# Kernel tuning notes

Hardware: AMD Instinct MI355X
Metric: run time of the kernel (lower is better)

## Reference

```python
import jax, jax.numpy as jnp
import numpy as np

B, S, D, H = 2, 2048, 1024, 16
DH = D // H
NEG = jnp.float32(-1e30)


def setup_inputs() -> dict:
    key = jax.random.key(0)
    ks = jax.random.split(key, 5)
    x = jax.random.normal(ks[0], (B, S, D), dtype=jnp.float32)
    # causal mask: attn_mask == 0 means blocked (matches masked_fill(attn_mask == 0))
    attn_mask = jnp.tril(jnp.ones((S, S), dtype=jnp.int32))
    key_padding_mask = jnp.zeros((B, S), dtype=bool)  # True = pad (none here)
    sd = 1.0 / np.sqrt(D)
    W_qkv = jax.random.normal(ks[1], (D, 3 * D), dtype=jnp.float32) * sd
    b_qkv = jnp.zeros((3 * D,), dtype=jnp.float32)
    W_proj = jax.random.normal(ks[2], (D, D), dtype=jnp.float32) * sd
    b_proj = jnp.zeros((D,), dtype=jnp.float32)
    return {"x": x, "W_qkv": W_qkv, "b_qkv": b_qkv, "W_proj": W_proj,
            "b_proj": b_proj, "attn_mask": attn_mask,
            "key_padding_mask": key_padding_mask}


def reference(x, W_qkv, b_qkv, W_proj, b_proj, attn_mask, key_padding_mask):
    scale = jnp.float32(DH) ** -0.5
    qkv = (x @ W_qkv + b_qkv).reshape(B, S, 3, H, DH)
    qkv = jnp.transpose(qkv, (2, 0, 3, 1, 4))  # (3, B, H, S, DH)
    q, k, v = qkv[0], qkv[1], qkv[2]
    attn = jnp.einsum("bhqd,bhkd->bhqk", q, k) * scale  # (B,H,S,S)
    # key padding mask: True -> -inf on that key column
    attn = jnp.where(key_padding_mask[:, None, None, :], NEG, attn)
    # attn mask: 0 -> blocked
    attn = jnp.where(attn_mask[None, None, :, :] == 0, NEG, attn)
    attn = jax.nn.softmax(attn, axis=-1)
    out = jnp.einsum("bhqk,bhkd->bhqd", attn, v)
    out = jnp.transpose(out, (0, 2, 1, 3)).reshape(B, S, D)
    return out @ W_proj + b_proj
```

## Files before the change

### kernel.cpp

```cpp
#include <hip/hip_runtime.h>


typedef __bf16 bf16;
typedef bf16 bf16x4 __attribute__((ext_vector_type(4)));
typedef bf16 bf16x8 __attribute__((ext_vector_type(8)));
typedef float f32x4 __attribute__((ext_vector_type(4)));

#define S_LEN 2048
#define DMODEL 1024
#define NHEAD 16
#define DHEAD 64

__device__ __forceinline__ void async_ld16(void* lds, const void* g) {
  __builtin_amdgcn_global_load_lds(
      (const __attribute__((address_space(1))) unsigned int*)g,
      (__attribute__((address_space(3))) unsigned int*)lds, 16, 0, 0);
}

__global__ __launch_bounds__(256) void prep_kernel(
    const float* __restrict__ x, const float* __restrict__ Wq,
    const float* __restrict__ Wp, bf16* __restrict__ Xb,
    bf16* __restrict__ Wtq, bf16* __restrict__ Wtp) {
  __shared__ float t[32][33];
  const int bid = blockIdx.x, tid = threadIdx.x;
  if (bid < 4096) {
    int i = bid * 256 + tid;
    float4 v = ((const float4*)x)[i];
    bf16x4 o;
    o[0] = (bf16)v.x; o[1] = (bf16)v.y; o[2] = (bf16)v.z; o[3] = (bf16)v.w;
    *(bf16x4*)(&Xb[4 * i]) = o;
    return;
  }
  const float* in; bf16* out; int R, C, bx, by;
  if (bid < 7168) {
    int b = bid - 4096; in = Wq; out = Wtq; R = 1024; C = 3072;
    bx = b % 96; by = b / 96;
  } else {
    int b = bid - 7168; in = Wp; out = Wtp; R = 1024; C = 1024;
    bx = b % 32; by = b / 32;
  }
  int tx = tid & 31, ty = tid >> 5;
  int bc = bx * 32, br = by * 32;
#pragma unroll
  for (int i = 0; i < 32; i += 8)
    t[ty + i][tx] = in[(size_t)(br + ty + i) * C + bc + tx];
  __syncthreads();
#pragma unroll
  for (int i = 0; i < 32; i += 8)
    out[(size_t)(bc + ty + i) * R + br + tx] = (bf16)t[tx][ty + i];
}

__global__ __launch_bounds__(512) void gemm_qkv(
    const bf16* __restrict__ A, const bf16* __restrict__ Bt,
    const float* __restrict__ bias, bf16* __restrict__ Oq,
    bf16* __restrict__ Ok, bf16* __restrict__ Ov, int Ksz) {
  __shared__ bf16 As[256 * 32];
  __shared__ bf16 Bs[128 * 32];
  const int tid = threadIdx.x, lane = tid & 63, w = tid >> 6;
  const int wm = (w >> 1) * 64, wn = (w & 1) * 64;
  const int lr = lane & 15, kg = lane >> 4;
  const int m0 = blockIdx.y * 256, n0 = blockIdx.x * 128;

  f32x4 acc[4][4] = {};

  bf16x8 areg[2], breg;
  const int ar0 = (tid) >> 2,        ac0 = (tid & 3) * 8;
  const int ar1 = (tid + 512) >> 2,  ac1 = ((tid + 512) & 3) * 8;
  const int br_ = tid >> 2,          bc_ = (tid & 3) * 8;

  areg[0] = *(const bf16x8*)(&A[(size_t)(m0 + ar0) * Ksz + ac0]);
  areg[1] = *(const bf16x8*)(&A[(size_t)(m0 + ar1) * Ksz + ac1]);
  breg    = *(const bf16x8*)(&Bt[(size_t)(n0 + br_) * Ksz + bc_]);

  for (int k0 = 0; k0 < Ksz; k0 += 32) {
    *(bf16x8*)(&As[ar0 * 32 + ac0]) = areg[0];
    *(bf16x8*)(&As[ar1 * 32 + ac1]) = areg[1];
    *(bf16x8*)(&Bs[br_ * 32 + bc_]) = breg;
    __syncthreads();

    if (k0 + 32 < Ksz) {
      const int kn = k0 + 32;
      areg[0] = *(const bf16x8*)(&A[(size_t)(m0 + ar0) * Ksz + kn + ac0]);
      areg[1] = *(const bf16x8*)(&A[(size_t)(m0 + ar1) * Ksz + kn + ac1]);
      breg    = *(const bf16x8*)(&Bt[(size_t)(n0 + br_) * Ksz + kn + bc_]);
    }

    bf16x8 af[4], bfr[4];
#pragma unroll
    for (int i = 0; i < 4; ++i)
      af[i] = *(const bf16x8*)(&As[(wm + i * 16 + lr) * 32 + kg * 8]);
#pragma unroll
    for (int j = 0; j < 4; ++j)
      bfr[j] = *(const bf16x8*)(&Bs[(wn + j * 16 + lr) * 32 + kg * 8]);
#pragma unroll
    for (int i = 0; i < 4; ++i)
#pragma unroll
      for (int j = 0; j < 4; ++j)
        acc[i][j] = __builtin_amdgcn_mfma_f32_16x16x32_bf16(af[i], bfr[j], acc[i][j], 0, 0, 0);
    __syncthreads();
  }

  const int rbase = kg * 4;
  const int t = n0 >> 10;
  if (t == 2) {
#pragma unroll
    for (int i = 0; i < 4; ++i) {
#pragma unroll
      for (int j = 0; j < 4; ++j) {
        int ncol = n0 + wn + j * 16 + lr;
        float bv = bias[ncol];
        int rem = ncol & 1023, h = rem >> 6, d = rem & 63;
        int m = m0 + wm + i * 16 + rbase;
        int s = m & 2047;
        size_t hb = (size_t)((m >> 11) * NHEAD + h) * S_LEN;
        bf16x4 pk;
#pragma unroll
        for (int r = 0; r < 4; ++r) pk[r] = (bf16)(acc[i][j][r] + bv);
        *(bf16x4*)(&Ov[hb * DHEAD + (size_t)d * S_LEN + s]) = pk;
      }
    }
  } else {
    bf16* Oqk = (t == 0) ? Oq : Ok;
#pragma unroll
    for (int i = 0; i < 4; ++i) {
#pragma unroll
      for (int j = 0; j < 4; ++j) {
        int ncol = n0 + wn + j * 16 + lr;
        float bv = bias[ncol];
        int rem = ncol & 1023, h = rem >> 6, d = rem & 63;
#pragma unroll
        for (int r = 0; r < 4; ++r) {
          int m = m0 + wm + i * 16 + rbase + r;
          int s = m & 2047;
          size_t hb = (size_t)((m >> 11) * NHEAD + h) * S_LEN;
          Oqk[(hb + s) * DHEAD + d] = (bf16)(acc[i][j][r] + bv);
        }
      }
    }
  }
}

__global__ __launch_bounds__(256) void gemm_proj(
    const bf16* __restrict__ A, const bf16* __restrict__ Bt,
    const float* __restrict__ bias, float* __restrict__ Of,
    int Ksz, int Nsz) {
  __shared__ bf16 As[64 * 32];
  __shared__ bf16 Bs[128 * 32];
  const int tid = threadIdx.x, lane = tid & 63, w = tid >> 6;
  const int wm = (w >> 1) * 32, wn = (w & 1) * 64;
  const int lr = lane & 15, kg = lane >> 4;
  const int m0 = blockIdx.y * 64, n0 = blockIdx.x * 128;

  f32x4 acc[2][4] = {};

  bf16x8 areg, breg[2];
  const int ar_ = tid >> 2,          ac_ = (tid & 3) * 8;
  const int br0 = tid >> 2,          bc0 = (tid & 3) * 8;
  const int br1 = (tid + 256) >> 2,  bc1 = ((tid + 256) & 3) * 8;

  areg    = *(const bf16x8*)(&A[(size_t)(m0 + ar_) * Ksz + ac_]);
  breg[0] = *(const bf16x8*)(&Bt[(size_t)(n0 + br0) * Ksz + bc0]);
  breg[1] = *(const bf16x8*)(&Bt[(size_t)(n0 + br1) * Ksz + bc1]);

  for (int k0 = 0; k0 < Ksz; k0 += 32) {
    *(bf16x8*)(&As[ar_ * 32 + ac_]) = areg;
    *(bf16x8*)(&Bs[br0 * 32 + bc0]) = breg[0];
    *(bf16x8*)(&Bs[br1 * 32 + bc1]) = breg[1];
    __syncthreads();

    if (k0 + 32 < Ksz) {
      const int kn = k0 + 32;
      areg    = *(const bf16x8*)(&A[(size_t)(m0 + ar_) * Ksz + kn + ac_]);
      breg[0] = *(const bf16x8*)(&Bt[(size_t)(n0 + br0) * Ksz + kn + bc0]);
      breg[1] = *(const bf16x8*)(&Bt[(size_t)(n0 + br1) * Ksz + kn + bc1]);
    }

    bf16x8 af[2], bfr[4];
#pragma unroll
    for (int i = 0; i < 2; ++i)
      af[i] = *(const bf16x8*)(&As[(wm + i * 16 + lr) * 32 + kg * 8]);
#pragma unroll
    for (int j = 0; j < 4; ++j)
      bfr[j] = *(const bf16x8*)(&Bs[(wn + j * 16 + lr) * 32 + kg * 8]);
#pragma unroll
    for (int i = 0; i < 2; ++i)
#pragma unroll
      for (int j = 0; j < 4; ++j)
        acc[i][j] = __builtin_amdgcn_mfma_f32_16x16x32_bf16(af[i], bfr[j], acc[i][j], 0, 0, 0);
    __syncthreads();
  }

  const int rbase = kg * 4;
#pragma unroll
  for (int i = 0; i < 2; ++i) {
#pragma unroll
    for (int j = 0; j < 4; ++j) {
      int ncol = n0 + wn + j * 16 + lr;
      float bv = bias[ncol];
#pragma unroll
      for (int r = 0; r < 4; ++r) {
        int m = m0 + wm + i * 16 + rbase + r;
        Of[(size_t)m * Nsz + ncol] = acc[i][j][r] + bv;
      }
    }
  }
}

__global__ __launch_bounds__(256) void attn_kernel(
    const bf16* __restrict__ Q, const bf16* __restrict__ K,
    const bf16* __restrict__ Vtg, bf16* __restrict__ O) {
  __shared__ bf16 Ks[128 * 72];
  __shared__ bf16 Vt[80 * 136];

  const int tid = threadIdx.x, lane = tid & 63, w = tid >> 6;
  const int lr = lane & 15, quad = lane >> 4;
  const int flat = blockIdx.x;
  const int p = (flat >> 3) & 15;
  const int bh = (flat & 7) + ((flat >> 7) << 3);
  const int b = bh >> 4, h = bh & 15;
  const bf16* Qp = Q + (size_t)bh * S_LEN * DHEAD;
  const bf16* Kp = K + (size_t)bh * S_LEN * DHEAD;
  const bf16* Vp = Vtg + (size_t)bh * S_LEN * DHEAD;

  for (int i = tid; i < 16 * 136; i += 256) {
    int rr = i / 136;
    Vt[(64 + rr) * 136 + (i - rr * 136)] = (rr == 0) ? (bf16)1.0f : (bf16)0.0f;
  }
  __syncthreads();

  const float qs = 0.125f * 1.44269504f;

  for (int seg = 0; seg < 2; ++seg) {
    const int qt = seg ? (31 - p) : p;
    const int q0 = qt * 64;
    const int qrow = q0 + w * 16;

    bf16x8 q0r = *(const bf16x8*)(Qp + (size_t)(qrow + lr) * DHEAD + quad * 8);
    bf16x8 q1r = *(const bf16x8*)(Qp + (size_t)(qrow + lr) * DHEAD + 32 + quad * 8);
    bf16x8 qf0, qf1;
#pragma unroll
    for (int e = 0; e < 8; ++e) {
      qf0[e] = (bf16)((float)q0r[e] * qs);
      qf1[e] = (bf16)((float)q1r[e] * qs);
    }

    f32x4 acc[4] = {};
    f32x4 acc5 = {};

    const int ktiles = (q0 + 63) / 128 + 1;

    bf16x8 kreg[4], vreg[4];
#pragma unroll
    for (int i = 0; i < 4; ++i) {
      int sg = tid + i * 256;
      int krow = sg >> 3, kc = (sg & 7) * 8;
      kreg[i] = *(const bf16x8*)(&Kp[(size_t)krow * DHEAD + kc]);
      int vd = sg >> 4, vs = (sg & 15) * 8;
      vreg[i] = *(const bf16x8*)(&Vp[(size_t)vd * S_LEN + vs]);
    }

    for (int kt = 0; kt < ktiles; ++kt) {
      const int kb = kt * 128;
#pragma unroll
      for (int i = 0; i < 4; ++i) {
        int sg = tid + i * 256;
        int krow = sg >> 3, kc = (sg & 7) * 8;
        int kl = krow & 31;
        int Rrow = (krow & ~31) | (((kl >> 2) & 1) << 4) | (((kl >> 3) & 3) << 2) | (kl & 3);
        *(bf16x8*)(&Ks[Rrow * 72 + kc]) = kreg[i];
        int vd = sg >> 4, vs = (sg & 15) * 8;
        *(bf16x8*)(&Vt[vd * 136 + vs]) = vreg[i];
      }
      __syncthreads();

      if (kt + 1 < ktiles) {
        const int kbn = kb + 128;
#pragma unroll
        for (int i = 0; i < 4; ++i) {
          int sg = tid + i * 256;
          int krow = sg >> 3, kc = (sg & 7) * 8;
          kreg[i] = *(const bf16x8*)(&Kp[(size_t)(kbn + krow) * DHEAD + kc]);
          int vd = sg >> 4, vs = (sg & 15) * 8;
          vreg[i] = *(const bf16x8*)(&Vp[(size_t)vd * S_LEN + kbn + vs]);
        }
      }

      f32x4 sc[8];
      __builtin_amdgcn_s_setprio(1);
#pragma unroll
      for (int ct = 0; ct < 8; ++ct) {
        bf16x8 kf0 = *(const bf16x8*)(&Ks[(ct * 16 + lr) * 72 + quad * 8]);
        bf16x8 kf1 = *(const bf16x8*)(&Ks[(ct * 16 + lr) * 72 + 32 + quad * 8]);
        f32x4 a = {};
        a = __builtin_amdgcn_mfma_f32_16x16x32_bf16(kf0, qf0, a, 0, 0, 0);
        a = __builtin_amdgcn_mfma_f32_16x16x32_bf16(kf1, qf1, a, 0, 0, 0);
        sc[ct] = a;
      }
      __builtin_amdgcn_s_setprio(0);

      if ((kb + 127) > qrow) {
        const int qg = qrow + lr;
#pragma unroll
        for (int ct = 0; ct < 8; ++ct)
#pragma unroll
          for (int r = 0; r < 4; ++r) {
            int key = kb + (ct >> 1) * 32 + quad * 8 + (ct & 1) * 4 + r;
            if (key > qg) sc[ct][r] = -1e30f;
          }
      }

      bf16x8 p8[4];
#pragma unroll
      for (int k0 = 0; k0 < 4; ++k0) {
        bf16x8 pf;
#pragma unroll
        for (int c = 0; c < 2; ++c)
#pragma unroll
          for (int r = 0; r < 4; ++r)
            pf[c * 4 + r] = (bf16)__builtin_amdgcn_exp2f(sc[2 * k0 + c][r]);
        p8[k0] = pf;
      }

      __builtin_amdgcn_s_setprio(1);
#pragma unroll
      for (int k0 = 0; k0 < 4; ++k0) {
#pragma unroll
        for (int nt = 0; nt < 4; ++nt) {
          bf16x8 vf = *(const bf16x8*)(&Vt[(nt * 16 + lr) * 136 + k0 * 32 + quad * 8]);
          acc[nt] = __builtin_amdgcn_mfma_f32_16x16x32_bf16(vf, p8[k0], acc[nt], 0, 0, 0);
        }
        bf16x8 vf5 = *(const bf16x8*)(&Vt[(64 + lr) * 136 + k0 * 32 + quad * 8]);
        acc5 = __builtin_amdgcn_mfma_f32_16x16x32_bf16(vf5, p8[k0], acc5, 0, 0, 0);
      }
      __builtin_amdgcn_s_setprio(0);
      __syncthreads();
    }

    float lsum = __shfl(acc5[0], lr);
    float inv = 1.f / lsum;
    size_t base = ((size_t)(b * S_LEN + qrow + lr)) * DMODEL + h * DHEAD;
#pragma unroll
    for (int nt = 0; nt < 4; ++nt) {
      bf16x4 ov;
#pragma unroll
      for (int r = 0; r < 4; ++r) ov[r] = (bf16)(acc[nt][r] * inv);
      *(bf16x4*)(&O[base + nt * 16 + quad * 4]) = ov;
    }
  }
}

extern "C" void kernel_launch(void* const* d_in, const int* in_sizes, int n_in,
                              void* d_out, int out_size, void* d_ws, size_t ws_size,
                              hipStream_t stream) {
  (void)in_sizes; (void)n_in; (void)out_size; (void)ws_size;
  const float* x     = (const float*)d_in[0];
  const float* Wqkv  = (const float*)d_in[1];
  const float* bqkv  = (const float*)d_in[2];
  const float* Wproj = (const float*)d_in[3];
  const float* bproj = (const float*)d_in[4];
  float* out = (float*)d_out;

  char* ws = (char*)d_ws;
  bf16* Xb  = (bf16*)(ws + 0);
  bf16* AO  = (bf16*)(ws + 0);
  bf16* Wtq = (bf16*)(ws + 8388608);
  bf16* Wtp = (bf16*)(ws + 16777216);
  bf16* Qb  = (bf16*)(ws + 18874368);
  bf16* Kb  = (bf16*)(ws + 27262976);
  bf16* Vtg = (bf16*)(ws + 35651584);

  prep_kernel<<<8192, 256, 0, stream>>>(x, Wqkv, Wproj, Xb, Wtq, Wtp);
  gemm_qkv<<<dim3(24, 16), 512, 0, stream>>>(Xb, Wtq, bqkv, Qb, Kb, Vtg, 1024);
  attn_kernel<<<512, 256, 0, stream>>>(Qb, Kb, Vtg, AO);
  gemm_proj<<<dim3(8, 64), 256, 0, stream>>>(AO, Wtp, bproj, out, 1024, 1024);
}
```

Baseline: 188.9 us.

## Double QKV GEMM K-tile to 64 and XOR-swizzle LDS layout

The QKV projection GEMM now stages 64-wide K slices instead of 32, halving the number of barrier-separated iterations. Shared-memory rows are stored with an XOR swizzle on 16-byte chunks to avoid bank conflicts on the 128-byte row stride. The change doubles LDS use and the prefetch register count per thread, which may reduce occupancy.

```diff
diff --git a/kernel.cpp b/kernel.cpp
--- a/kernel.cpp
+++ b/kernel.cpp
@@ -54,8 +54,8 @@
     const bf16* __restrict__ A, const bf16* __restrict__ Bt,
     const float* __restrict__ bias, bf16* __restrict__ Oq,
     bf16* __restrict__ Ok, bf16* __restrict__ Ov, int Ksz) {
-  __shared__ bf16 As[256 * 32];
-  __shared__ bf16 Bs[128 * 32];
+  __shared__ bf16 As[256 * 64];
+  __shared__ bf16 Bs[128 * 64];
   const int tid = threadIdx.x, lane = tid & 63, w = tid >> 6;
   const int wm = (w >> 1) * 64, wn = (w & 1) * 64;
   const int lr = lane & 15, kg = lane >> 4;
@@ -63,40 +63,62 @@
 
   f32x4 acc[4][4] = {};
 
-  bf16x8 areg[2], breg;
-  const int ar0 = (tid) >> 2,        ac0 = (tid & 3) * 8;
-  const int ar1 = (tid + 512) >> 2,  ac1 = ((tid + 512) & 3) * 8;
-  const int br_ = tid >> 2,          bc_ = (tid & 3) * 8;
-
-  areg[0] = *(const bf16x8*)(&A[(size_t)(m0 + ar0) * Ksz + ac0]);
-  areg[1] = *(const bf16x8*)(&A[(size_t)(m0 + ar1) * Ksz + ac1]);
-  breg    = *(const bf16x8*)(&Bt[(size_t)(n0 + br_) * Ksz + bc_]);
-
-  for (int k0 = 0; k0 < Ksz; k0 += 32) {
-    *(bf16x8*)(&As[ar0 * 32 + ac0]) = areg[0];
-    *(bf16x8*)(&As[ar1 * 32 + ac1]) = areg[1];
-    *(bf16x8*)(&Bs[br_ * 32 + bc_]) = breg;
+  bf16x8 areg[4], breg[2];
+  int arow[4], aslot[4], brow[2], bslot[2];
+#pragma unroll
+  for (int c = 0; c < 4; ++c) {
+    int g = tid + c * 512; arow[c] = g >> 3; aslot[c] = g & 7;
+  }
+#pragma unroll
+  for (int c = 0; c < 2; ++c) {
+    int g = tid + c * 512; brow[c] = g >> 3; bslot[c] = g & 7;
+  }
+
+#pragma unroll
+  for (int c = 0; c < 4; ++c)
+    areg[c] = *(const bf16x8*)(&A[(size_t)(m0 + arow[c]) * Ksz + aslot[c] * 8]);
+#pragma unroll
+  for (int c = 0; c < 2; ++c)
+    breg[c] = *(const bf16x8*)(&Bt[(size_t)(n0 + brow[c]) * Ksz + bslot[c] * 8]);
+
+  for (int k0 = 0; k0 < Ksz; k0 += 64) {
+#pragma unroll
+    for (int c = 0; c < 4; ++c)
+      *(bf16x8*)((char*)As + arow[c] * 128 + ((aslot[c] ^ (arow[c] & 7)) * 16)) = areg[c];
+#pragma unroll
+    for (int c = 0; c < 2; ++c)
+      *(bf16x8*)((char*)Bs + brow[c] * 128 + ((bslot[c] ^ (brow[c] & 7)) * 16)) = breg[c];
+
+    if (k0 + 64 < Ksz) {
+      const int kn = k0 + 64;
+#pragma unroll
+      for (int c = 0; c < 4; ++c)
+        areg[c] = *(const bf16x8*)(&A[(size_t)(m0 + arow[c]) * Ksz + kn + aslot[c] * 8]);
+#pragma unroll
+      for (int c = 0; c < 2; ++c)
+        breg[c] = *(const bf16x8*)(&Bt[(size_t)(n0 + brow[c]) * Ksz + kn + bslot[c] * 8]);
+    }
     __syncthreads();
 
-    if (k0 + 32 < Ksz) {
-      const int kn = k0 + 32;
-      areg[0] = *(const bf16x8*)(&A[(size_t)(m0 + ar0) * Ksz + kn + ac0]);
-      areg[1] = *(const bf16x8*)(&A[(size_t)(m0 + ar1) * Ksz + kn + ac1]);
-      breg    = *(const bf16x8*)(&Bt[(size_t)(n0 + br_) * Ksz + kn + bc_]);
-    }
-
-    bf16x8 af[4], bfr[4];
-#pragma unroll
-    for (int i = 0; i < 4; ++i)
-      af[i] = *(const bf16x8*)(&As[(wm + i * 16 + lr) * 32 + kg * 8]);
-#pragma unroll
-    for (int j = 0; j < 4; ++j)
-      bfr[j] = *(const bf16x8*)(&Bs[(wn + j * 16 + lr) * 32 + kg * 8]);
-#pragma unroll
-    for (int i = 0; i < 4; ++i)
-#pragma unroll
-      for (int j = 0; j < 4; ++j)
-        acc[i][j] = __builtin_amdgcn_mfma_f32_16x16x32_bf16(af[i], bfr[j], acc[i][j], 0, 0, 0);
+#pragma unroll
+    for (int h = 0; h < 2; ++h) {
+      bf16x8 af[4], bfr[4];
+#pragma unroll
+      for (int i = 0; i < 4; ++i) {
+        int row = wm + i * 16 + lr;
+        af[i] = *(const bf16x8*)((char*)As + row * 128 + (((h * 4 + kg) ^ (row & 7)) * 16));
+      }
+#pragma unroll
+      for (int j = 0; j < 4; ++j) {
+        int row = wn + j * 16 + lr;
+        bfr[j] = *(const bf16x8*)((char*)Bs + row * 128 + (((h * 4 + kg) ^ (row & 7)) * 16));
+      }
+#pragma unroll
+      for (int i = 0; i < 4; ++i)
+#pragma unroll
+        for (int j = 0; j < 4; ++j)
+          acc[i][j] = __builtin_amdgcn_mfma_f32_16x16x32_bf16(af[i], bfr[j], acc[i][j], 0, 0, 0);
+    }
     __syncthreads();
   }
 
```

Result: slower. 193.8 us (+2.6%).
